# Kernel optimization log

Hardware: AMD Instinct MI355X
Metric: run time of the kernel (lower is better)

The kernel has to match this reference:

```python
import jax, jax.numpy as jnp
import numpy as np


def setup_inputs() -> dict:
    key = jax.random.key(0)
    kx, ky = jax.random.split(key)
    x = jax.random.normal(kx, (4, 8192, 3), dtype=jnp.float32)
    y = jax.random.normal(ky, (4, 8192, 3), dtype=jnp.float32)
    return {"x": x, "y": y}


def _chamfer(x, y):
    # x: [B, N, D], y: [B, M, D]
    x2 = jnp.sum(x * x, axis=-1)                      # [B, N]
    y2 = jnp.sum(y * y, axis=-1)                      # [B, M]
    xy = jnp.einsum("bnd,bmd->bnm", x, y)             # [B, N, M]
    d2 = x2[:, :, None] + y2[:, None, :] - 2.0 * xy   # [B, N, M]
    d2 = jnp.maximum(d2, 0.0)
    cham_x = jnp.min(d2, axis=2).mean(axis=1)         # [B] min over M, mean over N
    cham_y = jnp.min(d2, axis=1).mean(axis=1)         # [B] min over N, mean over M
    return cham_x + cham_y                            # [B]


def reference(x, y):
    per_batch = _chamfer(x, y)
    return jnp.mean(per_batch)  # batch_reduction='mean'
```

## Files before the change

### kernel.cpp

```cpp
#include <hip/hip_runtime.h>


#define N_      8192
#define RPB     4096
#define NGRP    128
#define FLT_BIG 3.0e38f

typedef float v2f __attribute__((ext_vector_type(2)));

__global__ void zero_out_kernel(float* out) { *out = 0.0f; }

static __device__ __forceinline__ float rot16(float v) {
    return __uint_as_float((unsigned)__builtin_amdgcn_update_dpp(
        0, (int)__float_as_uint(v), 0x121, 0xf, 0xf, true));
}
static __device__ __forceinline__ v2f rot16v(v2f v) {
    v2f r; r.x = rot16(v.x); r.y = rot16(v.y); return r;
}

static __device__ __forceinline__ void do_record_v(
    v2f pxs, v2f pys, v2f pzs, v2f wv,
    const v2f* qx, const v2f* qy, const v2f* qz,
    float* acc)
{
    #pragma unroll
    for (int j = 0; j < 4; ++j) {
        v2f td, ts;
        asm("v_pk_fma_f32 %0, %1, %2, %3"
            : "=v"(td) : "v"(qz[j]), "v"(pzs), "v"(wv));
        asm("v_pk_fma_f32 %0, %1, %2, %3 op_sel:[0,1,1] op_sel_hi:[1,0,0]"
            : "=v"(ts) : "v"(qz[j]), "v"(pzs), "v"(wv));
        asm("v_pk_fma_f32 %0, %1, %2, %0"
            : "+v"(td) : "v"(qy[j]), "v"(pys));
        asm("v_pk_fma_f32 %0, %1, %2, %0 op_sel:[0,1,0] op_sel_hi:[1,0,1]"
            : "+v"(ts) : "v"(qy[j]), "v"(pys));
        asm("v_pk_fma_f32 %0, %1, %2, %0"
            : "+v"(td) : "v"(qx[j]), "v"(pxs));
        asm("v_pk_fma_f32 %0, %1, %2, %0 op_sel:[0,1,0] op_sel_hi:[1,0,1]"
            : "+v"(ts) : "v"(qx[j]), "v"(pxs));
        asm("v_min3_f32 %0, %0, %1, %2" : "+v"(acc[2*j])   : "v"(td.x), "v"(ts.x));
        asm("v_min3_f32 %0, %0, %1, %2" : "+v"(acc[2*j+1]) : "v"(td.y), "v"(ts.y));
    }
}

__global__ __launch_bounds__(512, 4) void chamfer_kernel(
    const float* __restrict__ xraw, const float* __restrict__ yraw,
    float* __restrict__ partial,
    unsigned int* __restrict__ ctrl,
    float* __restrict__ out)
{
    __shared__ float red[8 * 512];
    __shared__ unsigned int sflag;

    const int tid  = threadIdx.x;
    const int lane = tid & 63;
    const int wave = __builtin_amdgcn_readfirstlane(tid >> 6);
    const int blk  = blockIdx.x;
    const int dir   = blk >> 8;
    const int batch = (blk >> 6) & 3;
    const int qg    = (blk >> 2) & 15;
    const int seg   = blk & 3;
    const int g     = blk >> 2;

    const float* qraw = dir ? yraw : xraw;
    const float* oraw = dir ? xraw : yraw;

    const int qbase = batch * N_ + qg * 512;
    float f[24];
    {
        const float4* qv = (const float4*)(qraw + (size_t)qbase * 3) + lane * 6;
        #pragma unroll
        for (int k = 0; k < 6; ++k) {
            float4 t = qv[k];
            f[4*k] = t.x; f[4*k+1] = t.y; f[4*k+2] = t.z; f[4*k+3] = t.w;
        }
    }
    v2f qx[4], qy[4], qz[4];
    float acc[8];
    #pragma unroll
    for (int j = 0; j < 4; ++j) {
        qx[j] = (v2f){-2.0f * f[6*j+0], -2.0f * f[6*j+3]};
        qy[j] = (v2f){-2.0f * f[6*j+1], -2.0f * f[6*j+4]};
        qz[j] = (v2f){-2.0f * f[6*j+2], -2.0f * f[6*j+5]};
        acc[2*j] = FLT_BIG; acc[2*j+1] = FLT_BIG;
    }

    const float2* rp = (const float2*)
        (oraw + (size_t)(batch * RPB + seg * 1024 + wave * 128 + (lane & 15)) * 6);
    float2 A = rp[0], Bv = rp[1], Cv = rp[2];
    #pragma unroll 1
    for (int fl = 0; fl < 8; ++fl) {
        v2f pxs = (v2f){A.x,  Bv.y};
        v2f pys = (v2f){A.y,  Cv.x};
        v2f pzs = (v2f){Bv.x, Cv.y};
        v2f wv;
        wv.x = fmaf(A.x,  A.x,  fmaf(A.y,  A.y,  Bv.x * Bv.x));
        wv.y = fmaf(Bv.y, Bv.y, fmaf(Cv.x, Cv.x, Cv.y * Cv.y));
        if (fl < 7) {
            const float2* np = rp + (fl + 1) * 48;
            A = np[0]; Bv = np[1]; Cv = np[2];
        }
        #pragma unroll
        for (int s = 0; s < 16; ++s) {
            if (s) {
                pxs = rot16v(pxs); pys = rot16v(pys);
                pzs = rot16v(pzs); wv  = rot16v(wv);
            }
            do_record_v(pxs, pys, pzs, wv, qx, qy, qz, acc);
        }
    }

    #pragma unroll
    for (int j = 0; j < 8; ++j) red[wave * 512 + lane * 8 + j] = acc[j];
    __syncthreads();
    float m = red[tid];
    #pragma unroll
    for (int w = 1; w < 8; ++w) m = fminf(m, red[w * 512 + tid]);

    partial[((size_t)g * 4 + seg) * 512 + tid] = m;
    __syncthreads();
    if (tid == 0) {
        __threadfence();
        sflag = atomicAdd(&ctrl[g], 1u);
    }
    __syncthreads();
    if (sflag == 3u) {
        if (tid == 0) __threadfence();
        __syncthreads();
        const float* pg = partial + (size_t)g * 4 * 512;
        float mm = fminf(fminf(pg[tid], pg[512 + tid]),
                         fminf(pg[1024 + tid], pg[1536 + tid]));
        int gq = qbase + tid;
        float ax = qraw[gq*3+0], ay = qraw[gq*3+1], az = qraw[gq*3+2];
        float qn = fmaf(ax, ax, fmaf(ay, ay, az * az));
        float d2 = fmaxf(0.0f, qn + mm);
        #pragma unroll
        for (int o = 32; o > 0; o >>= 1) d2 += __shfl_xor(d2, o);
        if (lane == 0) red[wave] = d2;
        __syncthreads();
        if (tid == 0) {
            float s = red[0];
            #pragma unroll
            for (int w = 1; w < 8; ++w) s += red[w];
            atomicAdd((float*)&ctrl[NGRP + 1], s * (1.0f / 32768.0f));
            __threadfence();
            unsigned int o2 = atomicAdd(&ctrl[NGRP], 1u);
            if (o2 == (unsigned)(NGRP - 1)) {
                float tot = atomicAdd((float*)&ctrl[NGRP + 1], 0.0f);
                *out = tot;
            }
        }
    }
}

__global__ __launch_bounds__(1024) void chamfer_raw_kernel(
    const float* __restrict__ xraw, const float* __restrict__ yraw,
    float* __restrict__ out)
{
    __shared__ float4 red4[16][64];
    const int tid  = threadIdx.x;
    const int wave = tid >> 6;
    const int lane = tid & 63;
    const int blk  = blockIdx.x;
    const bool xdir = (blk < 128);
    const int b    = (blk & 127) >> 5;
    const int qofs = (blk & 31) << 8;
    const float* qraw = xdir ? xraw : yraw;
    const float* oraw = xdir ? yraw : xraw;
    float qx0[4], qx1[4], qx2[4], acc[4];
    #pragma unroll
    for (int q = 0; q < 4; ++q) {
        int gq = b * N_ + qofs + lane*4 + q;
        qx0[q] = qraw[gq*3+0]; qx1[q] = qraw[gq*3+1]; qx2[q] = qraw[gq*3+2];
        acc[q] = FLT_BIG;
    }
    const float* opp = oraw + (size_t)(b * N_ + wave * 512) * 3;
    #pragma unroll 4
    for (int k = 0; k < 512; ++k) {
        float p0 = opp[k*3+0], p1 = opp[k*3+1], p2 = opp[k*3+2];
        float w  = fmaf(p0, p0, fmaf(p1, p1, p2*p2));
        #pragma unroll
        for (int q = 0; q < 4; ++q) {
            float dot = qx0[q]*p0 + qx1[q]*p1 + qx2[q]*p2;
            acc[q] = fminf(acc[q], fmaf(-2.0f, dot, w));
        }
    }
    red4[wave][lane] = make_float4(acc[0], acc[1], acc[2], acc[3]);
    __syncthreads();
    if (tid < 256) {
        const float* red = (const float*)red4;
        float m = red[tid];
        #pragma unroll
        for (int w = 1; w < 16; ++w) m = fminf(m, red[w*256 + tid]);
        int gq = b * N_ + qofs + tid;
        float ax = qraw[gq*3+0], ay = qraw[gq*3+1], az = qraw[gq*3+2];
        float d2 = fmaxf(0.0f, fmaf(ax,ax,fmaf(ay,ay,az*az)) + m);
        #pragma unroll
        for (int off = 32; off > 0; off >>= 1) d2 += __shfl_xor(d2, off);
        if ((tid & 63) == 0) atomicAdd(out, d2 * (1.0f / 32768.0f));
    }
}

extern "C" void kernel_launch(void* const* d_in, const int* in_sizes, int n_in,
                              void* d_out, int out_size, void* d_ws, size_t ws_size,
                              hipStream_t stream)
{
    const float* x = (const float*)d_in[0];
    const float* y = (const float*)d_in[1];
    float* out = (float*)d_out;

    const size_t need = (size_t)NGRP * 4 * 512 * sizeof(float) + (NGRP + 2) * 4;
    if (ws_size >= need) {
        float* partial = (float*)d_ws;
        unsigned int* ctrl = (unsigned int*)(partial + (size_t)NGRP * 4 * 512);
        hipMemsetAsync(ctrl, 0, (NGRP + 2) * 4, stream);
        chamfer_kernel<<<512, 512, 0, stream>>>(x, y, partial, ctrl, out);
    } else {
        zero_out_kernel<<<1, 1, 0, stream>>>(out);
        chamfer_raw_kernel<<<256, 1024, 0, stream>>>(x, y, out);
    }
}
```

Measured before the change: 111.2 us.

## Compute both chamfer directions from one distance pass with column-min atomics

Each pairwise distance tile is now computed once and used for both the row minimum (x to y) and the column minimum (y to x). Query norms are added in-register and column minima are rotated along with the reference points, then reduced by lane shuffles. Results go into a global per-point min buffer through atomicMin on float bits. The grid is halved, and a separate sum kernel replaces the last-block reduction. This removes half of the distance arithmetic, but adds extra adds and min ops per pair, global atomics, and an extra memset and launch.

```diff
diff --git a/kernel.cpp b/kernel.cpp
--- a/kernel.cpp
+++ b/kernel.cpp
@@ -3,7 +3,6 @@
 
 #define N_      8192
 #define RPB     4096
-#define NGRP    128
 #define FLT_BIG 3.0e38f
 
 typedef float v2f __attribute__((ext_vector_type(2)));
@@ -18,10 +17,10 @@
     v2f r; r.x = rot16(v.x); r.y = rot16(v.y); return r;
 }
 
-static __device__ __forceinline__ void do_record_v(
+static __device__ __forceinline__ void do_record_sym(
     v2f pxs, v2f pys, v2f pzs, v2f wv,
-    const v2f* qx, const v2f* qy, const v2f* qz,
-    float* acc)
+    const v2f* qx, const v2f* qy, const v2f* qz, const v2f* qnv,
+    float* acc, v2f* cacc)
 {
     #pragma unroll
     for (int j = 0; j < 4; ++j) {
@@ -40,53 +39,56 @@
             : "+v"(ts) : "v"(qx[j]), "v"(pxs));
         asm("v_min3_f32 %0, %0, %1, %2" : "+v"(acc[2*j])   : "v"(td.x), "v"(ts.x));
         asm("v_min3_f32 %0, %0, %1, %2" : "+v"(acc[2*j+1]) : "v"(td.y), "v"(ts.y));
+        v2f tdq, tsq;
+        asm("v_pk_add_f32 %0, %1, %2" : "=v"(tdq) : "v"(td), "v"(qnv[j]));
+        asm("v_pk_add_f32 %0, %1, %2" : "=v"(tsq) : "v"(ts), "v"(qnv[j]));
+        asm("v_min3_f32 %0, %0, %1, %2" : "+v"(cacc->x) : "v"(tdq.x), "v"(tsq.y));
+        asm("v_min3_f32 %0, %0, %1, %2" : "+v"(cacc->y) : "v"(tsq.x), "v"(tdq.y));
     }
 }
 
 __global__ __launch_bounds__(512, 4) void chamfer_kernel(
     const float* __restrict__ xraw, const float* __restrict__ yraw,
-    float* __restrict__ partial,
-    unsigned int* __restrict__ ctrl,
-    float* __restrict__ out)
+    unsigned int* __restrict__ pmin)
 {
     __shared__ float red[8 * 512];
-    __shared__ unsigned int sflag;
+    __shared__ float colbuf[8][256];
 
     const int tid  = threadIdx.x;
     const int lane = tid & 63;
     const int wave = __builtin_amdgcn_readfirstlane(tid >> 6);
     const int blk  = blockIdx.x;
-    const int dir   = blk >> 8;
-    const int batch = (blk >> 6) & 3;
+    const int batch = blk >> 6;
     const int qg    = (blk >> 2) & 15;
     const int seg   = blk & 3;
-    const int g     = blk >> 2;
-
-    const float* qraw = dir ? yraw : xraw;
-    const float* oraw = dir ? xraw : yraw;
 
     const int qbase = batch * N_ + qg * 512;
     float f[24];
     {
-        const float4* qv = (const float4*)(qraw + (size_t)qbase * 3) + lane * 6;
+        const float4* qv = (const float4*)(xraw + (size_t)qbase * 3) + lane * 6;
         #pragma unroll
         for (int k = 0; k < 6; ++k) {
             float4 t = qv[k];
             f[4*k] = t.x; f[4*k+1] = t.y; f[4*k+2] = t.z; f[4*k+3] = t.w;
         }
     }
-    v2f qx[4], qy[4], qz[4];
+    v2f qx[4], qy[4], qz[4], qnv[4];
     float acc[8];
     #pragma unroll
     for (int j = 0; j < 4; ++j) {
+        qnv[j].x = fmaf(f[6*j+0], f[6*j+0],
+                   fmaf(f[6*j+1], f[6*j+1], f[6*j+2] * f[6*j+2]));
+        qnv[j].y = fmaf(f[6*j+3], f[6*j+3],
+                   fmaf(f[6*j+4], f[6*j+4], f[6*j+5] * f[6*j+5]));
         qx[j] = (v2f){-2.0f * f[6*j+0], -2.0f * f[6*j+3]};
         qy[j] = (v2f){-2.0f * f[6*j+1], -2.0f * f[6*j+4]};
         qz[j] = (v2f){-2.0f * f[6*j+2], -2.0f * f[6*j+5]};
         acc[2*j] = FLT_BIG; acc[2*j+1] = FLT_BIG;
     }
 
+    const int rbase = seg * 1024 + wave * 128;
     const float2* rp = (const float2*)
-        (oraw + (size_t)(batch * RPB + seg * 1024 + wave * 128 + (lane & 15)) * 6);
+        (yraw + (size_t)(batch * RPB + rbase + (lane & 15)) * 6);
     float2 A = rp[0], Bv = rp[1], Cv = rp[2];
     #pragma unroll 1
     for (int fl = 0; fl < 8; ++fl) {
@@ -100,13 +102,34 @@
             const float2* np = rp + (fl + 1) * 48;
             A = np[0]; Bv = np[1]; Cv = np[2];
         }
+        v2f cacc = (v2f){FLT_BIG, FLT_BIG};
         #pragma unroll
         for (int s = 0; s < 16; ++s) {
             if (s) {
                 pxs = rot16v(pxs); pys = rot16v(pys);
                 pzs = rot16v(pzs); wv  = rot16v(wv);
+                cacc = rot16v(cacc);
             }
-            do_record_v(pxs, pys, pzs, wv, qx, qy, qz, acc);
+            do_record_sym(pxs, pys, pzs, wv, qx, qy, qz, qnv, acc, &cacc);
+        }
+        cacc = rot16v(cacc);
+        cacc.x = fminf(cacc.x, __shfl_xor(cacc.x, 16));
+        cacc.x = fminf(cacc.x, __shfl_xor(cacc.x, 32));
+        cacc.y = fminf(cacc.y, __shfl_xor(cacc.y, 16));
+        cacc.y = fminf(cacc.y, __shfl_xor(cacc.y, 32));
+        if (lane < 16) {
+            colbuf[wave][fl * 32 + lane * 2]     = fmaxf(0.0f, cacc.x);
+            colbuf[wave][fl * 32 + lane * 2 + 1] = fmaxf(0.0f, cacc.y);
+        }
+    }
+
+    {
+        unsigned int* py = pmin + 32768 + batch * N_ + 2 * rbase;
+        #pragma unroll
+        for (int k = 0; k < 4; ++k) {
+            int idx = lane * 4 + k;
+            float v = colbuf[wave][idx];
+            atomicMin(&py[idx], __float_as_uint(v));
         }
     }
 
@@ -116,41 +139,22 @@
     float m = red[tid];
     #pragma unroll
     for (int w = 1; w < 8; ++w) m = fminf(m, red[w * 512 + tid]);
-
-    partial[((size_t)g * 4 + seg) * 512 + tid] = m;
-    __syncthreads();
-    if (tid == 0) {
-        __threadfence();
-        sflag = atomicAdd(&ctrl[g], 1u);
-    }
-    __syncthreads();
-    if (sflag == 3u) {
-        if (tid == 0) __threadfence();
-        __syncthreads();
-        const float* pg = partial + (size_t)g * 4 * 512;
-        float mm = fminf(fminf(pg[tid], pg[512 + tid]),
-                         fminf(pg[1024 + tid], pg[1536 + tid]));
-        int gq = qbase + tid;
-        float ax = qraw[gq*3+0], ay = qraw[gq*3+1], az = qraw[gq*3+2];
-        float qn = fmaf(ax, ax, fmaf(ay, ay, az * az));
-        float d2 = fmaxf(0.0f, qn + mm);
-        #pragma unroll
-        for (int o = 32; o > 0; o >>= 1) d2 += __shfl_xor(d2, o);
-        if (lane == 0) red[wave] = d2;
-        __syncthreads();
-        if (tid == 0) {
-            float s = red[0];
-            #pragma unroll
-            for (int w = 1; w < 8; ++w) s += red[w];
-            atomicAdd((float*)&ctrl[NGRP + 1], s * (1.0f / 32768.0f));
-            __threadfence();
-            unsigned int o2 = atomicAdd(&ctrl[NGRP], 1u);
-            if (o2 == (unsigned)(NGRP - 1)) {
-                float tot = atomicAdd((float*)&ctrl[NGRP + 1], 0.0f);
-                *out = tot;
-            }
-        }
-    }
+    int gq = qbase + tid;
+    float ax = xraw[gq*3+0], ay = xraw[gq*3+1], az = xraw[gq*3+2];
+    float qn = fmaf(ax, ax, fmaf(ay, ay, az * az));
+    float d2 = fmaxf(0.0f, qn + m);
+    atomicMin(&pmin[gq], __float_as_uint(d2));
+}
+
+__global__ __launch_bounds__(256) void sum_kernel(
+    const unsigned int* __restrict__ pmin, float* __restrict__ out)
+{
+    int i = blockIdx.x * 256 + threadIdx.x;
+    float4 v = ((const float4*)pmin)[i];
+    float s = v.x + v.y + v.z + v.w;
+    #pragma unroll
+    for (int off = 32; off > 0; off >>= 1) s += __shfl_xor(s, off);
+    if ((threadIdx.x & 63) == 0) atomicAdd(out, s * (1.0f / 32768.0f));
 }
 
 __global__ __launch_bounds__(1024) void chamfer_raw_kernel(
@@ -209,12 +213,13 @@
     const float* y = (const float*)d_in[1];
     float* out = (float*)d_out;
 
-    const size_t need = (size_t)NGRP * 4 * 512 * sizeof(float) + (NGRP + 2) * 4;
+    const size_t need = (size_t)65536 * 4;
     if (ws_size >= need) {
-        float* partial = (float*)d_ws;
-        unsigned int* ctrl = (unsigned int*)(partial + (size_t)NGRP * 4 * 512);
-        hipMemsetAsync(ctrl, 0, (NGRP + 2) * 4, stream);
-        chamfer_kernel<<<512, 512, 0, stream>>>(x, y, partial, ctrl, out);
+        unsigned int* pmin = (unsigned int*)d_ws;
+        hipMemsetAsync(pmin, 0xFF, need, stream);
+        hipMemsetAsync(out, 0, 4, stream);
+        chamfer_kernel<<<256, 512, 0, stream>>>(x, y, pmin);
+        sum_kernel<<<64, 256, 0, stream>>>(pmin, out);
     } else {
         zero_out_kernel<<<1, 1, 0, stream>>>(out);
         chamfer_raw_kernel<<<256, 1024, 0, stream>>>(x, y, out);
```

New measurement: 97.61 us. 1.14x faster.
